# Performance work log

Measured on AMD Instinct MI355X. Metric: run time of the kernel, lower is better.

The kernel has to match this reference:

```python
import jax, jax.numpy as jnp
import numpy as np

B, D, NB, NL, P, H = 65536, 256, 3, 2, 8, 4  # batch, d_model, n_banks, levels, prims/level, heads
HD = D // H


def setup_inputs() -> dict:
    key = jax.random.key(0)
    ks = jax.random.split(key, 8)
    z = jax.random.normal(ks[0], (B, D), dtype=jnp.float32)
    # per-bank hierarchical primitive embeddings [n_banks, n_levels, P, D]
    prims = jax.random.normal(ks[1], (NB, NL, P, D), dtype=jnp.float32) * 0.02
    level_weights = jnp.ones((NB, NL), dtype=jnp.float32) / NL
    # bank query projections, initialized to identity (nn.init.eye_)
    Wq = jnp.broadcast_to(jnp.eye(D, dtype=jnp.float32), (NB, D, D))
    # router gate (linear d_model -> n_banks)
    Wg = jax.random.normal(ks[2], (NB, D), dtype=jnp.float32) * 0.02
    bg = jnp.zeros((NB,), dtype=jnp.float32)
    # MultiheadAttention params (torch packed in_proj)
    in_proj_w = jax.random.normal(ks[3], (3 * D, D), dtype=jnp.float32) * 0.02
    in_proj_b = jnp.zeros((3 * D,), dtype=jnp.float32)
    out_w = jax.random.normal(ks[4], (D, D), dtype=jnp.float32) * 0.02
    out_b = jnp.zeros((D,), dtype=jnp.float32)
    ln_g = jnp.ones((D,), dtype=jnp.float32)
    ln_b = jnp.zeros((D,), dtype=jnp.float32)
    cross_attn_weight = jnp.array(0.5, dtype=jnp.float32)
    return {"z": z, "prims": prims, "level_weights": level_weights, "Wq": Wq,
            "Wg": Wg, "bg": bg, "in_proj_w": in_proj_w, "in_proj_b": in_proj_b,
            "out_w": out_w, "out_b": out_b, "ln_g": ln_g, "ln_b": ln_b,
            "cross_attn_weight": cross_attn_weight, "top_k": 2}


def _forward(z, prims, level_weights, Wq, Wg, bg, in_proj_w, in_proj_b,
             out_w, out_b, ln_g, ln_b, cross_attn_weight, top_k):
    b = z.shape[0]
    # ---- router: softmax gate + top-k sparse renormalization ----
    logits = z @ Wg.T + bg                              # [B, NB]
    probs = jax.nn.softmax(logits, axis=-1)
    topv, topi = jax.lax.top_k(probs, top_k)            # [B, k]
    routing = jnp.zeros_like(probs).at[jnp.arange(b)[:, None], topi].set(topv)
    routing = routing / (routing.sum(axis=-1, keepdims=True) + 1e-9)
    # ---- per-bank primitive attention (all banks computed, routed combine) ----
    query = jnp.einsum('bd,nod->bno', z, Wq)            # [B, NB, D]
    scores = jnp.einsum('bnd,nlpd->bnlp', query, prims) / jnp.sqrt(jnp.float32(D))
    alpha = jax.nn.softmax(scores, axis=-1)             # [B, NB, NL, P]
    level_out = jnp.einsum('bnlp,nlpd->bnld', alpha, prims)
    lw = jax.nn.softmax(level_weights, axis=-1)         # [NB, NL]
    bank_out = jnp.einsum('bnld,nl->bnd', level_out, lw)  # [B, NB, D]
    weighted = jnp.einsum('bn,bnd->bd', routing, bank_out)
    # ---- cross-bank MultiheadAttention: query z attends over NB bank tokens ----
    q = (z @ in_proj_w[:D].T + in_proj_b[:D]).reshape(b, H, HD)
    k = (bank_out @ in_proj_w[D:2 * D].T + in_proj_b[D:2 * D]).reshape(b, NB, H, HD)
    v = (bank_out @ in_proj_w[2 * D:].T + in_proj_b[2 * D:]).reshape(b, NB, H, HD)
    att = jnp.einsum('bhd,bnhd->bhn', q, k) / jnp.sqrt(jnp.float32(HD))
    att = jax.nn.softmax(att, axis=-1)
    attn_out = jnp.einsum('bhn,bnhd->bhd', att, v).reshape(b, D)
    attn_out = attn_out @ out_w.T + out_b
    # ---- gated mix + layernorm ----
    m = jax.nn.sigmoid(cross_attn_weight)
    y = (1.0 - m) * weighted + m * attn_out
    mu = y.mean(axis=-1, keepdims=True)
    var = y.var(axis=-1, keepdims=True)
    return (y - mu) / jnp.sqrt(var + 1e-5) * ln_g + ln_b


def reference(z, prims, level_weights, Wq, Wg, bg, in_proj_w, in_proj_b,
              out_w, out_b, ln_g, ln_b, cross_attn_weight, top_k):
    return _forward(z, prims, level_weights, Wq, Wg, bg, in_proj_w, in_proj_b,
                    out_w, out_b, ln_g, ln_b, cross_attn_weight, top_k)
```

## Files before the change

### kernel.cpp

```cpp
#include <hip/hip_runtime.h>

#define BD 256

#define WS_PQ   0
#define WS_MF   12288
#define WS_WZF  45056
#define WS_OB   77824
#define WS_BQK  78080
#define WS_LW   78336
#define WS_KP   78352
#define WS_VP   90640
#define WS_TOTAL 102928

typedef __bf16 bf16x8 __attribute__((ext_vector_type(8)));
typedef float  f32x4  __attribute__((ext_vector_type(4)));

__device__ __forceinline__ float bf2f(unsigned short u) {
  union { float f; unsigned int i; } c; c.i = ((unsigned int)u) << 16; return c.f;
}
__device__ __forceinline__ unsigned short f2bf(float f) {
  union { float f; unsigned int i; } c; c.f = f;
  unsigned int x = c.i;
  unsigned int r = (x + 0x7fffu + ((x >> 16) & 1u)) >> 16;
  return (unsigned short)r;
}
__device__ __forceinline__ int frag_idx(int k, int col) {
  return (((k >> 5) * 16 + (col >> 4)) * 64 + (((k >> 3) & 3) * 16 + (col & 15))) * 8 + (k & 7);
}

__global__ void hpm_pre1(const float* __restrict__ prims, const float* __restrict__ lvlw,
                         const float* __restrict__ wq, const float* __restrict__ ipw,
                         const float* __restrict__ ipb, const float* __restrict__ outw,
                         const float* __restrict__ outb, const float* __restrict__ caw,
                         float* __restrict__ ws) {
  int t = threadIdx.x, blk = blockIdx.x;
  float m = 1.0f / (1.0f + __expf(-caw[0]));
  if (blk < 96) {
    int nlp = (blk < 48) ? blk : blk - 48;
    const float4* pr = (const float4*)(prims + nlp * BD);
    const float4* wr = (const float4*)(ipw + (size_t)((blk < 48 ? 256 : 512) + t) * BD);
    float s0 = 0.f, s1 = 0.f, s2 = 0.f, s3 = 0.f;
#pragma unroll 8
    for (int i = 0; i < 64; ++i) {
      float4 p = pr[i], wv = wr[i];
      s0 = fmaf(p.x, wv.x, s0); s1 = fmaf(p.y, wv.y, s1);
      s2 = fmaf(p.z, wv.z, s2); s3 = fmaf(p.w, wv.w, s3);
    }
    ws[(blk < 48 ? WS_KP : WS_VP) + nlp * BD + t] = (s0 + s1) + (s2 + s3);
  } else if (blk < 144) {
    int nlp = blk - 96, n = nlp >> 4;
    const float* pr = prims + nlp * BD;
    const float* wqn = wq + (size_t)n * BD * BD + t;
    float s0 = 0.f, s1 = 0.f, s2 = 0.f, s3 = 0.f;
#pragma unroll 4
    for (int o = 0; o < BD; o += 4) {
      s0 = fmaf(pr[o + 0], wqn[(size_t)(o + 0) * BD], s0);
      s1 = fmaf(pr[o + 1], wqn[(size_t)(o + 1) * BD], s1);
      s2 = fmaf(pr[o + 2], wqn[(size_t)(o + 2) * BD], s2);
      s3 = fmaf(pr[o + 3], wqn[(size_t)(o + 3) * BD], s3);
    }
    ws[WS_PQ + nlp * BD + t] = ((s0 + s1) + (s2 + s3)) * (1.0f / 16.0f);
  } else {
    const float4* bv = (const float4*)(ipb + 512);
    const float4* orow = (const float4*)(outw + (size_t)t * BD);
    float s0 = 0.f, s1 = 0.f, s2 = 0.f, s3 = 0.f;
#pragma unroll 8
    for (int i = 0; i < 64; ++i) {
      float4 p = bv[i], wv = orow[i];
      s0 = fmaf(p.x, wv.x, s0); s1 = fmaf(p.y, wv.y, s1);
      s2 = fmaf(p.z, wv.z, s2); s3 = fmaf(p.w, wv.w, s3);
    }
    ws[WS_OB + t] = m * (((s0 + s1) + (s2 + s3)) + outb[t]);
    if (t == 0) {
      for (int n = 0; n < 3; ++n) {
        float a = lvlw[n * 2], b = lvlw[n * 2 + 1];
        float mx = fmaxf(a, b);
        float ea = __expf(a - mx), eb = __expf(b - mx);
        float inv = 1.0f / (ea + eb);
        ws[WS_LW + n * 2] = ea * inv;
        ws[WS_LW + n * 2 + 1] = eb * inv;
      }
      ws[WS_LW + 6] = 0.f; ws[WS_LW + 7] = 0.f;
    }
  }
}

__global__ void hpm_pre2(const float* __restrict__ prims, const float* __restrict__ wg,
                         const float* __restrict__ ipw, const float* __restrict__ ipb,
                         const float* __restrict__ outw, const float* __restrict__ caw,
                         float* __restrict__ ws) {
  int t = threadIdx.x, blk = blockIdx.x;
  float m = 1.0f / (1.0f + __expf(-caw[0]));
  unsigned short* WZ = (unsigned short*)(ws + WS_WZF);
  unsigned short* MF = (unsigned short*)(ws + WS_MF);
  if (blk < 192) {
    int h = blk / 48, nlp = blk % 48;
    const float* kpr = ws + WS_KP + nlp * BD + h * 64;
    const float* ip = ipw + (size_t)(h * 64) * BD + t;
    float s0 = 0.f, s1 = 0.f, s2 = 0.f, s3 = 0.f;
#pragma unroll 4
    for (int o = 0; o < 64; o += 4) {
      s0 = fmaf(ip[(size_t)(o + 0) * BD], kpr[o + 0], s0);
      s1 = fmaf(ip[(size_t)(o + 1) * BD], kpr[o + 1], s1);
      s2 = fmaf(ip[(size_t)(o + 2) * BD], kpr[o + 2], s2);
      s3 = fmaf(ip[(size_t)(o + 3) * BD], kpr[o + 3], s3);
    }
    WZ[frag_idx(t, 51 + h * 49 + nlp)] = f2bf(((s0 + s1) + (s2 + s3)) * 0.125f);
  } else if (blk < 196) {
    int h = blk - 192;
    const float* bk = ipb + 256 + h * 64;
    const float* ip = ipw + (size_t)(h * 64) * BD + t;
    float s = 0.f;
#pragma unroll 4
    for (int o = 0; o < 64; ++o) s = fmaf(ip[(size_t)o * BD], bk[o], s);
    WZ[frag_idx(t, 51 + h * 49 + 48)] = f2bf(s * 0.125f);
  } else if (blk < 388) {
    int q = blk - 196;
    int h = q / 48, nlp = q % 48;
    const float4* vp = (const float4*)(ws + WS_VP + nlp * BD + h * 64);
    const float4* orow = (const float4*)(outw + (size_t)t * BD + h * 64);
    float s0 = 0.f, s1 = 0.f, s2 = 0.f, s3 = 0.f;
#pragma unroll 8
    for (int i = 0; i < 16; ++i) {
      float4 p = vp[i], wv = orow[i];
      s0 = fmaf(p.x, wv.x, s0); s1 = fmaf(p.y, wv.y, s1);
      s2 = fmaf(p.z, wv.z, s2); s3 = fmaf(p.w, wv.w, s3);
    }
    MF[frag_idx(h * 48 + nlp, t)] = f2bf(m * ((s0 + s1) + (s2 + s3)));
  } else if (blk == 388) {
    if (t < 196) {
      int h = t / 49, j = t % 49;
      const float* bq = ipb + h * 64;
      float s = 0.f;
      if (j < 48) {
        const float* kpr = ws + WS_KP + j * BD + h * 64;
        for (int o = 0; o < 64; ++o) s = fmaf(bq[o], kpr[o], s);
      } else {
        const float* bk = ipb + 256 + h * 64;
        for (int o = 0; o < 64; ++o) s = fmaf(bq[o], bk[o], s);
      }
      ws[WS_BQK + h * 64 + j] = s * 0.125f;
    }
  } else if (blk < 440) {
    int col = blk - 389;
    float v = (col < 3) ? wg[col * BD + t] : ws[WS_PQ + (col - 3) * BD + t];
    WZ[frag_idx(t, col)] = f2bf(v);
  } else if (blk == 440) {
#pragma unroll
    for (int c = 247; c < 256; ++c) WZ[frag_idx(t, c)] = 0;
  } else if (blk < 489) {
    int i = blk - 441;
    MF[frag_idx(192 + i, t)] = f2bf((1.0f - m) * prims[i * BD + t]);
  } else {
    MF[frag_idx(240, t)] = f2bf(ws[WS_OB + t]);
#pragma unroll
    for (int k = 241; k < 256; ++k) MF[frag_idx(k, t)] = 0;
  }
}

__global__ __launch_bounds__(256) void hpm_main(
    const float* __restrict__ z, const float* __restrict__ wg,
    const float* __restrict__ bg, const float* __restrict__ lng,
    const float* __restrict__ lnb, const float* __restrict__ ws,
    float* __restrict__ out) {
  __shared__ unsigned short SB[16896];
  __shared__ float cbuf[32 * 48];
  __shared__ float rbuf[32 * 4];
  __shared__ float abuf[32 * 12];
  __shared__ float lred[32 * 8];
  __shared__ float lgb[512];

  const int tid = threadIdx.x;
  const int l = tid & 63;
  const int w = tid >> 6;
  const int l15 = l & 15, l16 = l >> 4;
  const int r0 = blockIdx.x * 32;

  lgb[tid] = lng[tid];
  lgb[256 + tid] = lnb[tid];

  {
    const int srow = tid >> 3, seg = tid & 7;
    const float* zr = z + (size_t)(r0 + srow) * BD + seg * 32;
    float l0 = 0.f, l1 = 0.f, l2 = 0.f;
    unsigned int pk[16];
#pragma unroll
    for (int j = 0; j < 8; ++j) {
      float4 zv = ((const float4*)zr)[j];
      const float* wgp = wg + seg * 32 + j * 4;
      float4 w0 = *(const float4*)(wgp);
      float4 w1 = *(const float4*)(wgp + BD);
      float4 w2 = *(const float4*)(wgp + 2 * BD);
      l0 = fmaf(zv.x, w0.x, fmaf(zv.y, w0.y, fmaf(zv.z, w0.z, fmaf(zv.w, w0.w, l0))));
      l1 = fmaf(zv.x, w1.x, fmaf(zv.y, w1.y, fmaf(zv.z, w1.z, fmaf(zv.w, w1.w, l1))));
      l2 = fmaf(zv.x, w2.x, fmaf(zv.y, w2.y, fmaf(zv.z, w2.z, fmaf(zv.w, w2.w, l2))));
      pk[j * 2 + 0] = (unsigned int)f2bf(zv.x) | ((unsigned int)f2bf(zv.y) << 16);
      pk[j * 2 + 1] = (unsigned int)f2bf(zv.z) | ((unsigned int)f2bf(zv.w) << 16);
    }
    unsigned short* zl = &SB[srow * 264 + seg * 32];
#pragma unroll
    for (int q = 0; q < 4; ++q)
      *(uint4*)(zl + q * 8) = make_uint4(pk[q * 4], pk[q * 4 + 1], pk[q * 4 + 2], pk[q * 4 + 3]);
#pragma unroll
    for (int mk = 1; mk < 8; mk <<= 1) {
      l0 += __shfl_xor(l0, mk, 64);
      l1 += __shfl_xor(l1, mk, 64);
      l2 += __shfl_xor(l2, mk, 64);
    }
    if (seg == 0) {
      l0 += bg[0]; l1 += bg[1]; l2 += bg[2];
      float mx = fmaxf(l0, fmaxf(l1, l2));
      float e0 = __expf(l0 - mx), e1 = __expf(l1 - mx), e2 = __expf(l2 - mx);
      float inv = 1.0f / (e0 + e1 + e2);
      float p0 = e0 * inv, p1 = e1 * inv, p2 = e2 * inv;
      int drop = (p2 <= p1 && p2 <= p0) ? 2 : ((p1 <= p0) ? 1 : 0);
      float a = (drop == 0) ? 0.f : p0;
      float b = (drop == 1) ? 0.f : p1;
      float c = (drop == 2) ? 0.f : p2;
      float den = 1.0f / (a + b + c + 1e-9f);
      rbuf[srow * 4 + 0] = a * den; rbuf[srow * 4 + 1] = b * den; rbuf[srow * 4 + 2] = c * den;
    }
  }
  __syncthreads();

  f32x4 zero4 = {0.f, 0.f, 0.f, 0.f};
  f32x4 acc[2][4];
#pragma unroll
  for (int rt = 0; rt < 2; ++rt)
#pragma unroll
    for (int j = 0; j < 4; ++j) acc[rt][j] = zero4;
  const uint4* wzf = (const uint4*)(ws + WS_WZF);
#pragma unroll
  for (int kt = 0; kt < 8; ++kt) {
    bf16x8 a0 = __builtin_bit_cast(bf16x8, *(const uint4*)&SB[l15 * 264 + kt * 32 + l16 * 8]);
    bf16x8 a1 = __builtin_bit_cast(bf16x8, *(const uint4*)&SB[(16 + l15) * 264 + kt * 32 + l16 * 8]);
#pragma unroll
    for (int j = 0; j < 4; ++j) {
      bf16x8 b = __builtin_bit_cast(bf16x8, wzf[(kt * 16 + (w * 4 + j)) * 64 + l]);
      acc[0][j] = __builtin_amdgcn_mfma_f32_16x16x32_bf16(a0, b, acc[0][j], 0, 0, 0);
      acc[1][j] = __builtin_amdgcn_mfma_f32_16x16x32_bf16(a1, b, acc[1][j], 0, 0, 0);
    }
  }
#pragma unroll
  for (int rt = 0; rt < 2; ++rt)
#pragma unroll
    for (int j = 0; j < 4; ++j)
#pragma unroll
      for (int r = 0; r < 4; ++r) {
        int row = rt * 16 + l16 * 4 + r;
        int col = (w * 4 + j) * 16 + l15;
        SB[8448 + row * 264 + col] = f2bf(acc[rt][j][r]);
      }
  __syncthreads();

  if (tid < 192) {
    int row = tid & 31, grp = tid >> 5;
    const unsigned short* tb = &SB[8448 + row * 264 + 3 + grp * 8];
    float sc[8]; float mx = -1e30f;
#pragma unroll
    for (int p = 0; p < 8; ++p) { sc[p] = bf2f(tb[p]); mx = fmaxf(mx, sc[p]); }
    float sum = 0.f;
#pragma unroll
    for (int p = 0; p < 8; ++p) { sc[p] = __expf(sc[p] - mx); sum += sc[p]; }
    float lwv = ws[WS_LW + grp] / sum;
#pragma unroll
    for (int p = 0; p < 8; ++p) cbuf[row * 48 + grp * 8 + p] = sc[p] * lwv;
  }
  __syncthreads();

  if (tid < 128) {
    int row = tid >> 2, h = tid & 3;
    const float* bq = ws + WS_BQK + h * 64;
    const unsigned short* tb = &SB[8448 + row * 264 + 51 + h * 49];
    float atk[3];
#pragma unroll
    for (int n = 0; n < 3; ++n) {
      float s = 0.f;
#pragma unroll
      for (int i = 0; i < 16; ++i)
        s = fmaf(cbuf[row * 48 + n * 16 + i], bf2f(tb[n * 16 + i]) + bq[n * 16 + i], s);
      atk[n] = s;
    }
    float cb = bf2f(tb[48]) + bq[48];
    float a0 = atk[0] + cb, a1 = atk[1] + cb, a2 = atk[2] + cb;
    float mx = fmaxf(a0, fmaxf(a1, a2));
    float e0 = __expf(a0 - mx), e1 = __expf(a1 - mx), e2 = __expf(a2 - mx);
    float inv = 1.0f / (e0 + e1 + e2);
    abuf[(row * 4 + h) * 3 + 0] = e0 * inv;
    abuf[(row * 4 + h) * 3 + 1] = e1 * inv;
    abuf[(row * 4 + h) * 3 + 2] = e2 * inv;
  }
  __syncthreads();

  if (tid < 128) {
    int row = tid >> 2, h = tid & 3;
    int xr = (row & 7) << 3;
    int base = row * 256;
    const float* cb = cbuf + row * 48;
    const float* ab = abuf + (row * 4 + h) * 3;
#pragma unroll
    for (int g = 0; g < 6; ++g) {
      float an = ab[g >> 1];
      unsigned int ph[4], pl[4];
#pragma unroll
      for (int q2 = 0; q2 < 4; ++q2) {
        float g0 = an * cb[g * 8 + q2 * 2 + 0];
        float g1 = an * cb[g * 8 + q2 * 2 + 1];
        unsigned short h0 = f2bf(g0), h1 = f2bf(g1);
        unsigned short e0 = f2bf(g0 - bf2f(h0)), e1 = f2bf(g1 - bf2f(h1));
        ph[q2] = (unsigned int)h0 | ((unsigned int)h1 << 16);
        pl[q2] = (unsigned int)e0 | ((unsigned int)e1 << 16);
      }
      int k0 = (h * 48 + g * 8) ^ xr;
      *(uint4*)&SB[base + k0] = make_uint4(ph[0], ph[1], ph[2], ph[3]);
      *(uint4*)&SB[8192 + base + k0] = make_uint4(pl[0], pl[1], pl[2], pl[3]);
    }
  } else if (tid < 160) {
    int row = tid - 128;
    int xr = (row & 7) << 3;
    int base = row * 256;
    const float* cb = cbuf + row * 48;
    const float* rb = rbuf + row * 4;
#pragma unroll
    for (int g = 0; g < 6; ++g) {
      float rn = rb[g >> 1];
      unsigned int ph[4], pl[4];
#pragma unroll
      for (int q2 = 0; q2 < 4; ++q2) {
        float g0 = rn * cb[g * 8 + q2 * 2 + 0];
        float g1 = rn * cb[g * 8 + q2 * 2 + 1];
        unsigned short h0 = f2bf(g0), h1 = f2bf(g1);
        unsigned short e0 = f2bf(g0 - bf2f(h0)), e1 = f2bf(g1 - bf2f(h1));
        ph[q2] = (unsigned int)h0 | ((unsigned int)h1 << 16);
        pl[q2] = (unsigned int)e0 | ((unsigned int)e1 << 16);
      }
      int k0 = (192 + g * 8) ^ xr;
      *(uint4*)&SB[base + k0] = make_uint4(ph[0], ph[1], ph[2], ph[3]);
      *(uint4*)&SB[8192 + base + k0] = make_uint4(pl[0], pl[1], pl[2], pl[3]);
    }
    int k240 = 240 ^ xr;
    *(uint4*)&SB[base + k240] = make_uint4(0x3f80u, 0u, 0u, 0u);
    *(uint4*)&SB[8192 + base + k240] = make_uint4(0u, 0u, 0u, 0u);
    int k248 = 248 ^ xr;
    *(uint4*)&SB[base + k248] = make_uint4(0u, 0u, 0u, 0u);
    *(uint4*)&SB[8192 + base + k248] = make_uint4(0u, 0u, 0u, 0u);
  }
  __syncthreads();

  f32x4 acc3[2][4];
#pragma unroll
  for (int rt = 0; rt < 2; ++rt)
#pragma unroll
    for (int j = 0; j < 4; ++j) acc3[rt][j] = zero4;
  const uint4* mf = (const uint4*)(ws + WS_MF);
#pragma unroll
  for (int kt = 0; kt < 8; ++kt) {
    uint4 uah[2], ual[2];
#pragma unroll
    for (int rt = 0; rt < 2; ++rt) {
      int row = rt * 16 + l15;
      int hidx = row * 256 + ((kt * 32 + l16 * 8) ^ ((row & 7) << 3));
      uah[rt] = *(const uint4*)&SB[hidx];
      ual[rt] = *(const uint4*)&SB[8192 + hidx];
    }
#pragma unroll
    for (int j = 0; j < 4; ++j) {
      bf16x8 b = __builtin_bit_cast(bf16x8, mf[(kt * 16 + w * 4 + j) * 64 + l]);
#pragma unroll
      for (int rt = 0; rt < 2; ++rt) {
        acc3[rt][j] = __builtin_amdgcn_mfma_f32_16x16x32_bf16(__builtin_bit_cast(bf16x8, uah[rt]), b, acc3[rt][j], 0, 0, 0);
        acc3[rt][j] = __builtin_amdgcn_mfma_f32_16x16x32_bf16(__builtin_bit_cast(bf16x8, ual[rt]), b, acc3[rt][j], 0, 0, 0);
      }
    }
  }

  float sm[2][4], sq[2][4];
#pragma unroll
  for (int rt = 0; rt < 2; ++rt)
#pragma unroll
    for (int r = 0; r < 4; ++r) {
      float s = 0.f, q2 = 0.f;
#pragma unroll
      for (int j = 0; j < 4; ++j) { float v = acc3[rt][j][r]; s += v; q2 = fmaf(v, v, q2); }
      sm[rt][r] = s; sq[rt][r] = q2;
    }
#pragma unroll
  for (int mk = 1; mk < 16; mk <<= 1)
#pragma unroll
    for (int rt = 0; rt < 2; ++rt)
#pragma unroll
      for (int r = 0; r < 4; ++r) {
        sm[rt][r] += __shfl_xor(sm[rt][r], mk, 64);
        sq[rt][r] += __shfl_xor(sq[rt][r], mk, 64);
      }
  if (l15 == 0) {
#pragma unroll
    for (int rt = 0; rt < 2; ++rt)
#pragma unroll
      for (int r = 0; r < 4; ++r) {
        int row = rt * 16 + l16 * 4 + r;
        lred[(row * 4 + w) * 2 + 0] = sm[rt][r];
        lred[(row * 4 + w) * 2 + 1] = sq[rt][r];
      }
  }
  __syncthreads();
#pragma unroll
  for (int rt = 0; rt < 2; ++rt)
#pragma unroll
    for (int r = 0; r < 4; ++r) {
      int row = rt * 16 + l16 * 4 + r;
      float ts = lred[(row * 4 + 0) * 2] + lred[(row * 4 + 1) * 2] + lred[(row * 4 + 2) * 2] + lred[(row * 4 + 3) * 2];
      float tq = lred[(row * 4 + 0) * 2 + 1] + lred[(row * 4 + 1) * 2 + 1] + lred[(row * 4 + 2) * 2 + 1] + lred[(row * 4 + 3) * 2 + 1];
      float mu = ts * (1.0f / 256.0f);
      float var = tq * (1.0f / 256.0f) - mu * mu;
      float rstd = rsqrtf(var + 1e-5f);
#pragma unroll
      for (int j = 0; j < 4; ++j) {
        int col = (w * 4 + j) * 16 + l15;
        float v = (acc3[rt][j][r] - mu) * rstd * lgb[col] + lgb[256 + col];
        out[(size_t)(r0 + row) * BD + col] = v;
      }
    }
}

extern "C" void kernel_launch(void* const* d_in, const int* in_sizes, int n_in,
                              void* d_out, int out_size, void* d_ws, size_t ws_size,
                              hipStream_t stream) {
  const float* z     = (const float*)d_in[0];
  const float* prims = (const float*)d_in[1];
  const float* lvlw  = (const float*)d_in[2];
  const float* wq    = (const float*)d_in[3];
  const float* wg    = (const float*)d_in[4];
  const float* bg    = (const float*)d_in[5];
  const float* ipw   = (const float*)d_in[6];
  const float* ipb   = (const float*)d_in[7];
  const float* outw  = (const float*)d_in[8];
  const float* outb  = (const float*)d_in[9];
  const float* lng   = (const float*)d_in[10];
  const float* lnb   = (const float*)d_in[11];
  const float* caw   = (const float*)d_in[12];
  float* wsf = (float*)d_ws;
  float* out = (float*)d_out;

  if (ws_size < (size_t)WS_TOTAL * sizeof(float)) return;

  const int B = in_sizes[0] / BD;
  hpm_pre1<<<145, 256, 0, stream>>>(prims, lvlw, wq, ipw, ipb, outw, outb, caw, wsf);
  hpm_pre2<<<490, 256, 0, stream>>>(prims, wg, ipw, ipb, outw, caw, wsf);
  hpm_main<<<B / 32, 256, 0, stream>>>(z, wg, bg, lng, lnb, wsf, out);
}
```

Before: 212.6 us.

## Halve shared-memory buffer by building hi/lo bf16 split in two sequential passes

The shared buffer SB is cut from 16896 to 8448 shorts. The scores tile now reuses the front of the buffer, and the hi and lo bf16 parts of the G matrix are built and multiplied in two separate passes over the same region instead of living side by side. This lowers LDS use per block, and the launch bound now asks for 5 blocks per CU, so occupancy should rise. The cost is two extra barriers, the G construction running twice, and the MF weight fragments being reloaded from global memory for the second pass.

```diff
diff --git a/kernel.cpp b/kernel.cpp
--- a/kernel.cpp
+++ b/kernel.cpp
@@ -158,12 +158,66 @@
   }
 }
 
-__global__ __launch_bounds__(256) void hpm_main(
+template<int LO>
+__device__ __forceinline__ void build_G(unsigned short* SB, const float* cbuf,
+                                        const float* rbuf, const float* abuf, int tid) {
+  if (tid < 128) {
+    int row = tid >> 2, h = tid & 3;
+    int xr = (row & 7) << 3;
+    int base = row * 256;
+    const float* cb = cbuf + row * 48;
+    const float* ab = abuf + (row * 4 + h) * 3;
+#pragma unroll
+    for (int g = 0; g < 6; ++g) {
+      float an = ab[g >> 1];
+      unsigned int pk[4];
+#pragma unroll
+      for (int q2 = 0; q2 < 4; ++q2) {
+        float g0 = an * cb[g * 8 + q2 * 2 + 0];
+        float g1 = an * cb[g * 8 + q2 * 2 + 1];
+        unsigned short v0, v1;
+        if (LO) { v0 = f2bf(g0 - bf2f(f2bf(g0))); v1 = f2bf(g1 - bf2f(f2bf(g1))); }
+        else    { v0 = f2bf(g0);                  v1 = f2bf(g1); }
+        pk[q2] = (unsigned int)v0 | ((unsigned int)v1 << 16);
+      }
+      int k0 = (h * 48 + g * 8) ^ xr;
+      *(uint4*)&SB[base + k0] = make_uint4(pk[0], pk[1], pk[2], pk[3]);
+    }
+  } else if (tid < 160) {
+    int row = tid - 128;
+    int xr = (row & 7) << 3;
+    int base = row * 256;
+    const float* cb = cbuf + row * 48;
+    const float* rb = rbuf + row * 4;
+#pragma unroll
+    for (int g = 0; g < 6; ++g) {
+      float rn = rb[g >> 1];
+      unsigned int pk[4];
+#pragma unroll
+      for (int q2 = 0; q2 < 4; ++q2) {
+        float g0 = rn * cb[g * 8 + q2 * 2 + 0];
+        float g1 = rn * cb[g * 8 + q2 * 2 + 1];
+        unsigned short v0, v1;
+        if (LO) { v0 = f2bf(g0 - bf2f(f2bf(g0))); v1 = f2bf(g1 - bf2f(f2bf(g1))); }
+        else    { v0 = f2bf(g0);                  v1 = f2bf(g1); }
+        pk[q2] = (unsigned int)v0 | ((unsigned int)v1 << 16);
+      }
+      int k0 = (192 + g * 8) ^ xr;
+      *(uint4*)&SB[base + k0] = make_uint4(pk[0], pk[1], pk[2], pk[3]);
+    }
+    int k240 = 240 ^ xr;
+    *(uint4*)&SB[base + k240] = make_uint4(LO ? 0u : 0x3f80u, 0u, 0u, 0u);
+    int k248 = 248 ^ xr;
+    *(uint4*)&SB[base + k248] = make_uint4(0u, 0u, 0u, 0u);
+  }
+}
+
+__global__ __launch_bounds__(256, 5) void hpm_main(
     const float* __restrict__ z, const float* __restrict__ wg,
     const float* __restrict__ bg, const float* __restrict__ lng,
     const float* __restrict__ lnb, const float* __restrict__ ws,
     float* __restrict__ out) {
-  __shared__ unsigned short SB[16896];
+  __shared__ unsigned short SB[8448];
   __shared__ float cbuf[32 * 48];
   __shared__ float rbuf[32 * 4];
   __shared__ float abuf[32 * 12];
@@ -241,6 +295,8 @@
       acc[1][j] = __builtin_amdgcn_mfma_f32_16x16x32_bf16(a1, b, acc[1][j], 0, 0, 0);
     }
   }
+  __syncthreads();
+
 #pragma unroll
   for (int rt = 0; rt < 2; ++rt)
 #pragma unroll
@@ -249,13 +305,13 @@
       for (int r = 0; r < 4; ++r) {
         int row = rt * 16 + l16 * 4 + r;
         int col = (w * 4 + j) * 16 + l15;
-        SB[8448 + row * 264 + col] = f2bf(acc[rt][j][r]);
+        SB[row * 264 + col] = f2bf(acc[rt][j][r]);
       }
   __syncthreads();
 
   if (tid < 192) {
     int row = tid & 31, grp = tid >> 5;
-    const unsigned short* tb = &SB[8448 + row * 264 + 3 + grp * 8];
+    const unsigned short* tb = &SB[row * 264 + 3 + grp * 8];
     float sc[8]; float mx = -1e30f;
 #pragma unroll
     for (int p = 0; p < 8; ++p) { sc[p] = bf2f(tb[p]); mx = fmaxf(mx, sc[p]); }
@@ -271,7 +327,7 @@
   if (tid < 128) {
     int row = tid >> 2, h = tid & 3;
     const float* bq = ws + WS_BQK + h * 64;
-    const unsigned short* tb = &SB[8448 + row * 264 + 51 + h * 49];
+    const unsigned short* tb = &SB[row * 264 + 51 + h * 49];
     float atk[3];
 #pragma unroll
     for (int n = 0; n < 3; ++n) {
@@ -292,85 +348,48 @@
   }
   __syncthreads();
 
-  if (tid < 128) {
-    int row = tid >> 2, h = tid & 3;
-    int xr = (row & 7) << 3;
-    int base = row * 256;
-    const float* cb = cbuf + row * 48;
-    const float* ab = abuf + (row * 4 + h) * 3;
-#pragma unroll
-    for (int g = 0; g < 6; ++g) {
-      float an = ab[g >> 1];
-      unsigned int ph[4], pl[4];
-#pragma unroll
-      for (int q2 = 0; q2 < 4; ++q2) {
-        float g0 = an * cb[g * 8 + q2 * 2 + 0];
-        float g1 = an * cb[g * 8 + q2 * 2 + 1];
-        unsigned short h0 = f2bf(g0), h1 = f2bf(g1);
-        unsigned short e0 = f2bf(g0 - bf2f(h0)), e1 = f2bf(g1 - bf2f(h1));
-        ph[q2] = (unsigned int)h0 | ((unsigned int)h1 << 16);
-        pl[q2] = (unsigned int)e0 | ((unsigned int)e1 << 16);
-      }
-      int k0 = (h * 48 + g * 8) ^ xr;
-      *(uint4*)&SB[base + k0] = make_uint4(ph[0], ph[1], ph[2], ph[3]);
-      *(uint4*)&SB[8192 + base + k0] = make_uint4(pl[0], pl[1], pl[2], pl[3]);
-    }
-  } else if (tid < 160) {
-    int row = tid - 128;
-    int xr = (row & 7) << 3;
-    int base = row * 256;
-    const float* cb = cbuf + row * 48;
-    const float* rb = rbuf + row * 4;
-#pragma unroll
-    for (int g = 0; g < 6; ++g) {
-      float rn = rb[g >> 1];
-      unsigned int ph[4], pl[4];
-#pragma unroll
-      for (int q2 = 0; q2 < 4; ++q2) {
-        float g0 = rn * cb[g * 8 + q2 * 2 + 0];
-        float g1 = rn * cb[g * 8 + q2 * 2 + 1];
-        unsigned short h0 = f2bf(g0), h1 = f2bf(g1);
-        unsigned short e0 = f2bf(g0 - bf2f(h0)), e1 = f2bf(g1 - bf2f(h1));
-        ph[q2] = (unsigned int)h0 | ((unsigned int)h1 << 16);
-        pl[q2] = (unsigned int)e0 | ((unsigned int)e1 << 16);
-      }
-      int k0 = (192 + g * 8) ^ xr;
-      *(uint4*)&SB[base + k0] = make_uint4(ph[0], ph[1], ph[2], ph[3]);
-      *(uint4*)&SB[8192 + base + k0] = make_uint4(pl[0], pl[1], pl[2], pl[3]);
-    }
-    int k240 = 240 ^ xr;
-    *(uint4*)&SB[base + k240] = make_uint4(0x3f80u, 0u, 0u, 0u);
-    *(uint4*)&SB[8192 + base + k240] = make_uint4(0u, 0u, 0u, 0u);
-    int k248 = 248 ^ xr;
-    *(uint4*)&SB[base + k248] = make_uint4(0u, 0u, 0u, 0u);
-    *(uint4*)&SB[8192 + base + k248] = make_uint4(0u, 0u, 0u, 0u);
-  }
-  __syncthreads();
-
   f32x4 acc3[2][4];
 #pragma unroll
   for (int rt = 0; rt < 2; ++rt)
 #pragma unroll
     for (int j = 0; j < 4; ++j) acc3[rt][j] = zero4;
   const uint4* mf = (const uint4*)(ws + WS_MF);
+
+  build_G<0>(SB, cbuf, rbuf, abuf, tid);
+  __syncthreads();
 #pragma unroll
   for (int kt = 0; kt < 8; ++kt) {
-    uint4 uah[2], ual[2];
+    uint4 ua[2];
 #pragma unroll
     for (int rt = 0; rt < 2; ++rt) {
       int row = rt * 16 + l15;
-      int hidx = row * 256 + ((kt * 32 + l16 * 8) ^ ((row & 7) << 3));
-      uah[rt] = *(const uint4*)&SB[hidx];
-      ual[rt] = *(const uint4*)&SB[8192 + hidx];
+      ua[rt] = *(const uint4*)&SB[row * 256 + ((kt * 32 + l16 * 8) ^ ((row & 7) << 3))];
     }
 #pragma unroll
     for (int j = 0; j < 4; ++j) {
       bf16x8 b = __builtin_bit_cast(bf16x8, mf[(kt * 16 + w * 4 + j) * 64 + l]);
 #pragma unroll
-      for (int rt = 0; rt < 2; ++rt) {
-        acc3[rt][j] = __builtin_amdgcn_mfma_f32_16x16x32_bf16(__builtin_bit_cast(bf16x8, uah[rt]), b, acc3[rt][j], 0, 0, 0);
-        acc3[rt][j] = __builtin_amdgcn_mfma_f32_16x16x32_bf16(__builtin_bit_cast(bf16x8, ual[rt]), b, acc3[rt][j], 0, 0, 0);
-      }
+      for (int rt = 0; rt < 2; ++rt)
+        acc3[rt][j] = __builtin_amdgcn_mfma_f32_16x16x32_bf16(__builtin_bit_cast(bf16x8, ua[rt]), b, acc3[rt][j], 0, 0, 0);
+    }
+  }
+  __syncthreads();
+  build_G<1>(SB, cbuf, rbuf, abuf, tid);
+  __syncthreads();
+#pragma unroll
+  for (int kt = 0; kt < 8; ++kt) {
+    uint4 ua[2];
+#pragma unroll
+    for (int rt = 0; rt < 2; ++rt) {
+      int row = rt * 16 + l15;
+      ua[rt] = *(const uint4*)&SB[row * 256 + ((kt * 32 + l16 * 8) ^ ((row & 7) << 3))];
+    }
+#pragma unroll
+    for (int j = 0; j < 4; ++j) {
+      bf16x8 b = __builtin_bit_cast(bf16x8, mf[(kt * 16 + w * 4 + j) * 64 + l]);
+#pragma unroll
+      for (int rt = 0; rt < 2; ++rt)
+        acc3[rt][j] = __builtin_amdgcn_mfma_f32_16x16x32_bf16(__builtin_bit_cast(bf16x8, ua[rt]), b, acc3[rt][j], 0, 0, 0);
     }
   }
 
```

Result: slower. 273.8 us (+28.8%).
